# Performance work log

Measured on AMD Instinct MI355X. Metric: run time of the kernel, lower is better.

The kernel has to match this reference:

```python
import jax, jax.numpy as jnp
import numpy as np

B, N, S, D, ITERS = 128, 8192, 4, 32, 3
LN_EPS = 1e-5

def _ln(x, g, b):
    m = jnp.mean(x, axis=-1, keepdims=True)
    v = jnp.mean((x - m) ** 2, axis=-1, keepdims=True)
    return (x - m) * jax.lax.rsqrt(v + LN_EPS) * g + b

def setup_inputs() -> dict:
    key = jax.random.key(0)
    ks = jax.random.split(key, 16)
    s = 1.0 / np.sqrt(D)
    return {
        "x": jax.random.normal(ks[0], (B, N, D), jnp.float32),
        "slot_noise": jax.random.normal(ks[1], (B, S, D), jnp.float32),
        "slots_mu": jax.random.normal(ks[2], (1, 1, D), jnp.float32),
        "slots_logsigma": jnp.zeros((1, 1, D), jnp.float32),
        "Wq": jax.random.uniform(ks[3], (D, D), jnp.float32, -s, s),
        "Wk": jax.random.uniform(ks[4], (D, D), jnp.float32, -s, s),
        "Wv": jax.random.uniform(ks[5], (D, D), jnp.float32, -s, s),
        "gru_Wih": jax.random.uniform(ks[6], (3 * D, D), jnp.float32, -s, s),
        "gru_Whh": jax.random.uniform(ks[7], (3 * D, D), jnp.float32, -s, s),
        "gru_bih": jax.random.uniform(ks[8], (3 * D,), jnp.float32, -s, s),
        "gru_bhh": jax.random.uniform(ks[9], (3 * D,), jnp.float32, -s, s),
        "mlp_W1": jax.random.uniform(ks[10], (D, D), jnp.float32, -s, s),
        "mlp_b1": jax.random.uniform(ks[11], (D,), jnp.float32, -s, s),
        "mlp_W2": jax.random.uniform(ks[12], (D, D), jnp.float32, -s, s),
        "mlp_b2": jax.random.uniform(ks[13], (D,), jnp.float32, -s, s),
        "lnx_g": jnp.ones((D,), jnp.float32), "lnx_b": jnp.zeros((D,), jnp.float32),
        "lns_g": jnp.ones((D,), jnp.float32), "lns_b": jnp.zeros((D,), jnp.float32),
        "lnff_g": jnp.ones((D,), jnp.float32), "lnff_b": jnp.zeros((D,), jnp.float32),
    }

def reference(x, slot_noise, slots_mu, slots_logsigma, Wq, Wk, Wv,
              gru_Wih, gru_Whh, gru_bih, gru_bhh,
              mlp_W1, mlp_b1, mlp_W2, mlp_b2,
              lnx_g, lnx_b, lns_g, lns_b, lnff_g, lnff_b):
    d = x.shape[-1]
    scale = d ** (-0.5)
    xn = _ln(x, lnx_g, lnx_b)                      # [B,N,D]
    k = xn @ Wk.T                                  # [B,N,D] (x fixed -> hoist out of loop)
    v = xn @ Wv.T
    slots = slots_mu + slot_noise * jnp.exp(slots_logsigma)  # [B,S,D]
    for _ in range(ITERS):
        q = _ln(slots, lns_g, lns_b) @ Wq.T        # [B,S,D]
        attn = jnp.einsum('bsd,bnd->bsn', q, k) * scale
        attn = jax.nn.softmax(attn, axis=-1) + 1e-8
        attn = attn / jnp.sum(attn, axis=-1, keepdims=True)
        upd = jnp.einsum('bsn,bnd->bsd', attn, v)  # [B,S,D]
        # GRUCell (PyTorch gate order: r, z, n)
        gi = upd @ gru_Wih.T + gru_bih             # [B,S,3D]
        gh = slots @ gru_Whh.T + gru_bhh
        ir, iz, inn = jnp.split(gi, 3, axis=-1)
        hr, hz, hn = jnp.split(gh, 3, axis=-1)
        r = jax.nn.sigmoid(ir + hr)
        z = jax.nn.sigmoid(iz + hz)
        n = jnp.tanh(inn + r * hn)
        slots = (1.0 - z) * n + z * slots
        h = jax.nn.relu(_ln(slots, lnff_g, lnff_b) @ mlp_W1.T + mlp_b1)
        slots = slots + (h @ mlp_W2.T + mlp_b2)
    return slots.reshape(slots.shape[0], -1)
```

## Files before the change

kernel.cpp:

```cpp
#include <hip/hip_runtime.h>
#include <hip/hip_bf16.h>


#define Bn 128
#define Nn 8192
#define Sn 4
#define Dn 32
#define SCALE 0.17677669529663687f
#define RENORM (1.0f / (1.0f + (float)Nn * 1e-8f))

#define Cn 8
#define RPB (Nn / Cn)
#define PT 256
#define RSTEP 128
#define NSTEP (RPB / RSTEP)

#define WS_REQ ((size_t)(3 * Bn * Sn * Dn + 3 * Bn * Cn * Sn * Dn + 6 * Bn * Cn * Sn) * 4)

__device__ __forceinline__ float sigmoidf_(float v) { return 1.0f / (1.0f + __expf(-v)); }

template<int KIND, int WANT_QT>
__device__ __forceinline__ void chain_fn(
    int b, int tid,
    const float* __restrict__ pa_prev, const float* __restrict__ pb_prev,
    const float* __restrict__ ps_prev,
    const float* __restrict__ slots_prev,
    const float* __restrict__ noise, const float* __restrict__ mu,
    const float* __restrict__ logsig,
    const float* __restrict__ lnx_g, const float* __restrict__ lnx_b,
    const float* __restrict__ Wv,
    const float* __restrict__ Wih, const float* __restrict__ Whh,
    const float* __restrict__ bih, const float* __restrict__ bhh,
    const float* __restrict__ W1, const float* __restrict__ b1v,
    const float* __restrict__ W2, const float* __restrict__ b2v,
    const float* __restrict__ lns_g, const float* __restrict__ lns_b,
    const float* __restrict__ lnff_g, const float* __restrict__ lnff_b,
    const float* __restrict__ Wq, const float* __restrict__ Wk,
    float (*qt_sh)[Dn], float (*ta)[Dn], float (*tb)[Dn],
    float* __restrict__ store)
{
    const int s = (tid >> 5) & 3, d = tid & 31;
    const bool act = tid < 128;
    float sfin = 0.f;

    if constexpr (KIND == 0) {
        if (act)
            sfin = mu[d] + noise[(b * Sn + s) * Dn + d] * __expf(logsig[d]);
    } else {
        float sv_c = 0.f, lnffv = 0.f;
        if (act) {
            float PA = 0.f, PB = 0.f, PS = 0.f;
            #pragma unroll
            for (int c = 0; c < Cn; ++c) {
                PA += pa_prev[(((size_t)b * Cn + c) * Sn + s) * Dn + d];
                PB += pb_prev[((size_t)b * Cn + c) * Sn + s];
                PS += ps_prev[((size_t)b * Cn + c) * Sn + s];
            }
            float u = fmaf(lnx_g[d], PA - PB, PS * lnx_b[d]);
            ta[s][d] = (u / PS) * RENORM;
            tb[s][d] = slots_prev[(b * Sn + s) * Dn + d];
        }
        __syncthreads();
        float updv = 0.f;
        if (act) {
            #pragma unroll 8
            for (int j = 0; j < 32; ++j) updv = fmaf(Wv[d * 32 + j], ta[s][j], updv);
        }
        __syncthreads();
        if (act) ta[s][d] = updv;
        __syncthreads();
        if (act) {
            float gi[3], gh[3];
            #pragma unroll
            for (int g3 = 0; g3 < 3; ++g3) {
                const int row = g3 * 32 + d;
                float a1 = bih[row], a2 = bhh[row];
                #pragma unroll 8
                for (int j = 0; j < 32; ++j) {
                    a1 = fmaf(Wih[row * 32 + j], ta[s][j], a1);
                    a2 = fmaf(Whh[row * 32 + j], tb[s][j], a2);
                }
                gi[g3] = a1; gh[g3] = a2;
            }
            float r  = sigmoidf_(gi[0] + gh[0]);
            float z  = sigmoidf_(gi[1] + gh[1]);
            float nn = tanhf(gi[2] + r * gh[2]);
            sv_c = (1.0f - z) * nn + z * tb[s][d];
            float sx = sv_c, sxx = sv_c * sv_c;
            #pragma unroll
            for (int m = 1; m <= 16; m <<= 1) { sx += __shfl_xor(sx, m); sxx += __shfl_xor(sxx, m); }
            float mean = sx * (1.0f / 32.0f);
            float var  = sxx * (1.0f / 32.0f) - mean * mean;
            lnffv = (sv_c - mean) * rsqrtf(var + 1e-5f) * lnff_g[d] + lnff_b[d];
        }
        __syncthreads();
        if (act) ta[s][d] = lnffv;
        __syncthreads();
        if (act) {
            float h = b1v[d];
            #pragma unroll 8
            for (int j = 0; j < 32; ++j) h = fmaf(W1[d * 32 + j], ta[s][j], h);
            tb[s][d] = fmaxf(h, 0.f);
        }
        __syncthreads();
        if (act) {
            float o = b2v[d];
            #pragma unroll 8
            for (int j = 0; j < 32; ++j) o = fmaf(W2[d * 32 + j], tb[s][j], o);
            sfin = sv_c + o;
        }
    }

    if (act && store) store[(b * Sn + s) * Dn + d] = sfin;

    if constexpr (WANT_QT) {
        float lnsv = 0.f;
        if (act) {
            float sx = sfin, sxx = sfin * sfin;
            #pragma unroll
            for (int m = 1; m <= 16; m <<= 1) { sx += __shfl_xor(sx, m); sxx += __shfl_xor(sxx, m); }
            float mean = sx * (1.0f / 32.0f);
            float var  = sxx * (1.0f / 32.0f) - mean * mean;
            lnsv = (sfin - mean) * rsqrtf(var + 1e-5f) * lns_g[d] + lns_b[d];
        }
        __syncthreads();
        if (act) ta[s][d] = lnsv;
        __syncthreads();
        if (act) {
            float q = 0.f;
            #pragma unroll 8
            for (int j = 0; j < 32; ++j) q = fmaf(Wq[d * 32 + j], ta[s][j], q);
            tb[s][d] = q;
        }
        __syncthreads();
        if (act) {
            float qv = 0.f;
            #pragma unroll 8
            for (int i = 0; i < 32; ++i) qv = fmaf(tb[s][i], Wk[i * 32 + d], qv);
            qt_sh[s][d] = qv * SCALE;
        }
        __syncthreads();
    }
}

template<int IT>
__global__ __launch_bounds__(PT)
void pass_k(const float* __restrict__ x,
            const float* __restrict__ noise, const float* __restrict__ mu,
            const float* __restrict__ logsig,
            const float* __restrict__ Wq, const float* __restrict__ Wk,
            const float* __restrict__ Wv,
            const float* __restrict__ Wih, const float* __restrict__ Whh,
            const float* __restrict__ bih, const float* __restrict__ bhh,
            const float* __restrict__ W1, const float* __restrict__ b1v,
            const float* __restrict__ W2, const float* __restrict__ b2v,
            const float* __restrict__ lnx_g, const float* __restrict__ lnx_b,
            const float* __restrict__ lns_g, const float* __restrict__ lns_b,
            const float* __restrict__ lnff_g, const float* __restrict__ lnff_b,
            const float* __restrict__ slots_prev, float* __restrict__ slots_cur,
            const float* __restrict__ pa_prev, const float* __restrict__ pb_prev,
            const float* __restrict__ ps_prev,
            float* __restrict__ pa_cur, float* __restrict__ pb_cur,
            float* __restrict__ ps_cur)
{
    const int c = blockIdx.x, b = blockIdx.y, tid = threadIdx.x;
    __shared__ float qt_sh[Sn][Dn], ta[Sn][Dn], tb[Sn][Dn];
    __shared__ float ls_pa[4][Sn][Dn];
    __shared__ float ls_pb[4][Sn];
    __shared__ float ls_ps[4][Sn];

    chain_fn<(IT == 0 ? 0 : 1), 1>(b, tid, pa_prev, pb_prev, ps_prev, slots_prev,
        noise, mu, logsig, lnx_g, lnx_b, Wv, Wih, Whh, bih, bhh, W1, b1v, W2, b2v,
        lns_g, lns_b, lnff_g, lnff_b, Wq, Wk,
        qt_sh, ta, tb, (c == 0) ? slots_cur : nullptr);

    const int sub = tid & 3, col0 = sub * 8, rg = tid >> 2;

    float qg[4][8], qgs[4], qe[4];
    {
        float g8[8], e8[8];
        #pragma unroll
        for (int k = 0; k < 8; ++k) { g8[k] = lnx_g[col0 + k]; e8[k] = lnx_b[col0 + k]; }
        #pragma unroll
        for (int s = 0; s < 4; ++s) {
            float sg = 0.f, se = 0.f;
            #pragma unroll
            for (int k = 0; k < 8; ++k) {
                float q = qt_sh[s][col0 + k];
                qg[s][k] = q * g8[k];
                sg += qg[s][k];
                se = fmaf(q, e8[k], se);
            }
            sg += __shfl_xor(sg, 1); sg += __shfl_xor(sg, 2);
            se += __shfl_xor(se, 1); se += __shfl_xor(se, 2);
            qgs[s] = sg; qe[s] = se;
        }
    }

    float pa[4][8], pb[4] = {0.f,0.f,0.f,0.f}, ps[4] = {0.f,0.f,0.f,0.f};
    #pragma unroll
    for (int s = 0; s < 4; ++s)
        #pragma unroll
        for (int k = 0; k < 8; ++k) pa[s][k] = 0.f;

    const float* xb = x + ((size_t)b * Nn + (size_t)c * RPB) * Dn;
    const float* pA0 = xb + (size_t)rg * Dn + col0;
    const float* pB0 = pA0 + 64 * Dn;
    float4 a0 = *(const float4*)(pA0);
    float4 a1 = *(const float4*)(pA0 + 4);
    float4 b0 = *(const float4*)(pB0);
    float4 b1 = *(const float4*)(pB0 + 4);

    for (int t = 0; t < NSTEP; ++t) {
        const int tn = (t + 1 < NSTEP) ? t + 1 : t;
        const float* qA = xb + (size_t)(tn * RSTEP + rg) * Dn + col0;
        const float* qB = qA + 64 * Dn;
        float4 nA0 = *(const float4*)(qA);
        float4 nA1 = *(const float4*)(qA + 4);
        float4 nB0 = *(const float4*)(qB);
        float4 nB1 = *(const float4*)(qB + 4);

        float xA[8] = {a0.x, a0.y, a0.z, a0.w, a1.x, a1.y, a1.z, a1.w};
        float xB[8] = {b0.x, b0.y, b0.z, b0.w, b1.x, b1.y, b1.z, b1.w};

        float sxA = 0.f, sxxA = 0.f, dA[4] = {0.f,0.f,0.f,0.f};
        float sxB = 0.f, sxxB = 0.f, dB[4] = {0.f,0.f,0.f,0.f};
        #pragma unroll
        for (int k = 0; k < 8; ++k) {
            sxA += xA[k];  sxxA = fmaf(xA[k], xA[k], sxxA);
            sxB += xB[k];  sxxB = fmaf(xB[k], xB[k], sxxB);
            #pragma unroll
            for (int s = 0; s < 4; ++s) {
                dA[s] = fmaf(xA[k], qg[s][k], dA[s]);
                dB[s] = fmaf(xB[k], qg[s][k], dB[s]);
            }
        }
        sxA += __shfl_xor(sxA, 1); sxxA += __shfl_xor(sxxA, 1);
        sxB += __shfl_xor(sxB, 1); sxxB += __shfl_xor(sxxB, 1);
        #pragma unroll
        for (int s = 0; s < 4; ++s) { dA[s] += __shfl_xor(dA[s], 1); dB[s] += __shfl_xor(dB[s], 1); }
        sxA += __shfl_xor(sxA, 2); sxxA += __shfl_xor(sxxA, 2);
        sxB += __shfl_xor(sxB, 2); sxxB += __shfl_xor(sxxB, 2);
        #pragma unroll
        for (int s = 0; s < 4; ++s) { dA[s] += __shfl_xor(dA[s], 2); dB[s] += __shfl_xor(dB[s], 2); }

        float meanA = sxA * (1.0f / 32.0f);
        float varA  = sxxA * (1.0f / 32.0f) - meanA * meanA;
        float rsA   = rsqrtf(varA + 1e-5f);
        float meanB = sxB * (1.0f / 32.0f);
        float varB  = sxxB * (1.0f / 32.0f) - meanB * meanB;
        float rsB   = rsqrtf(varB + 1e-5f);

        #pragma unroll
        for (int s = 0; s < 4; ++s) {
            float lgA = fmaf(rsA, fmaf(-meanA, qgs[s], dA[s]), qe[s]);
            float lgB = fmaf(rsB, fmaf(-meanB, qgs[s], dB[s]), qe[s]);
            float wA = __expf(lgA), wB = __expf(lgB);
            float alA = wA * rsA,  alB = wB * rsB;
            ps[s] += wA + wB;
            pb[s] = fmaf(alA, meanA, fmaf(alB, meanB, pb[s]));
            #pragma unroll
            for (int k = 0; k < 8; ++k)
                pa[s][k] = fmaf(alA, xA[k], fmaf(alB, xB[k], pa[s][k]));
        }
        a0 = nA0; a1 = nA1; b0 = nB0; b1 = nB1;
    }

    #pragma unroll
    for (int m = 4; m <= 32; m <<= 1) {
        #pragma unroll
        for (int s = 0; s < 4; ++s) {
            ps[s] += __shfl_xor(ps[s], m);
            pb[s] += __shfl_xor(pb[s], m);
            #pragma unroll
            for (int k = 0; k < 8; ++k) pa[s][k] += __shfl_xor(pa[s][k], m);
        }
    }

    const int wv = tid >> 6, lane = tid & 63;
    if (lane < 4) {
        #pragma unroll
        for (int s = 0; s < 4; ++s)
            #pragma unroll
            for (int k = 0; k < 8; ++k) ls_pa[wv][s][lane * 8 + k] = pa[s][k];
        if (lane == 0) {
            #pragma unroll
            for (int s = 0; s < 4; ++s) { ls_pb[wv][s] = pb[s]; ls_ps[wv][s] = ps[s]; }
        }
    }
    __syncthreads();
    if (tid < 128) {
        const int s = tid >> 5, d = tid & 31;
        float a = ls_pa[0][s][d] + ls_pa[1][s][d] + ls_pa[2][s][d] + ls_pa[3][s][d];
        pa_cur[(((size_t)b * Cn + c) * Sn + s) * Dn + d] = a;
        if (d == 0) {
            pb_cur[((size_t)b * Cn + c) * Sn + s] =
                ls_pb[0][s] + ls_pb[1][s] + ls_pb[2][s] + ls_pb[3][s];
            ps_cur[((size_t)b * Cn + c) * Sn + s] =
                ls_ps[0][s] + ls_ps[1][s] + ls_ps[2][s] + ls_ps[3][s];
        }
    }
}

__global__ __launch_bounds__(128)
void final_k(const float* __restrict__ lnx_g, const float* __restrict__ lnx_b,
             const float* __restrict__ Wv,
             const float* __restrict__ Wih, const float* __restrict__ Whh,
             const float* __restrict__ bih, const float* __restrict__ bhh,
             const float* __restrict__ W1, const float* __restrict__ b1v,
             const float* __restrict__ W2, const float* __restrict__ b2v,
             const float* __restrict__ lns_g, const float* __restrict__ lns_b,
             const float* __restrict__ lnff_g, const float* __restrict__ lnff_b,
             const float* __restrict__ Wq, const float* __restrict__ Wk,
             const float* __restrict__ slots_prev,
             const float* __restrict__ pa_prev, const float* __restrict__ pb_prev,
             const float* __restrict__ ps_prev,
             float* __restrict__ out)
{
    const int b = blockIdx.x, tid = threadIdx.x;
    __shared__ float qt_sh[Sn][Dn], ta[Sn][Dn], tb[Sn][Dn];
    chain_fn<1, 0>(b, tid, pa_prev, pb_prev, ps_prev, slots_prev,
        nullptr, nullptr, nullptr, lnx_g, lnx_b,
        Wv, Wih, Whh, bih, bhh, W1, b1v, W2, b2v,
        lns_g, lns_b, lnff_g, lnff_b, Wq, Wk, qt_sh, ta, tb, out);
}

#define TPB 1024
#define NW (TPB / 64)
#define RPS (TPB / 4)
#define STEPS (Nn / RPS)

__global__ __launch_bounds__(TPB)
void slot_fused(const float* __restrict__ x, const float* __restrict__ noise,
                const float* __restrict__ mu, const float* __restrict__ logsig,
                const float* __restrict__ Wq, const float* __restrict__ Wk,
                const float* __restrict__ Wv,
                const float* __restrict__ Wih, const float* __restrict__ Whh,
                const float* __restrict__ bih, const float* __restrict__ bhh,
                const float* __restrict__ W1, const float* __restrict__ b1v,
                const float* __restrict__ W2, const float* __restrict__ b2v,
                const float* __restrict__ lnx_g, const float* __restrict__ lnx_b,
                const float* __restrict__ lns_g, const float* __restrict__ lns_b,
                const float* __restrict__ lnff_g, const float* __restrict__ lnff_b,
                float* __restrict__ out)
{
    const int b   = blockIdx.x;
    const int tid = threadIdx.x;
    __shared__ float slots_sh[Sn][Dn];
    __shared__ float qt_sh[Sn][Dn];
    __shared__ float a_sh[Sn][Dn];
    __shared__ float b_sh[Sn][Dn];
    __shared__ float h_sh[Sn][Dn];
    __shared__ float ls_u[NW][Sn][Dn];
    __shared__ float ls_s[NW][Sn];
    const int s128 = tid >> 5, d128 = tid & 31;

    if (tid < 128) {
        float sv = mu[d128] + noise[(b * Sn + s128) * Dn + d128] * __expf(logsig[d128]);
        slots_sh[s128][d128] = sv;
        float sx = sv, sxx = sv * sv;
        #pragma unroll
        for (int m = 1; m <= 16; m <<= 1) { sx += __shfl_xor(sx, m); sxx += __shfl_xor(sxx, m); }
        float mean = sx * (1.0f / 32.0f);
        float var  = sxx * (1.0f / 32.0f) - mean * mean;
        a_sh[s128][d128] = (sv - mean) * rsqrtf(var + 1e-5f) * lns_g[d128] + lns_b[d128];
    }
    __syncthreads();
    if (tid < 128) {
        float q = 0.f;
        #pragma unroll 8
        for (int j = 0; j < 32; ++j) q = fmaf(Wq[d128 * 32 + j], a_sh[s128][j], q);
        b_sh[s128][d128] = q;
    }
    __syncthreads();
    if (tid < 128) {
        float qv = 0.f;
        #pragma unroll 8
        for (int i = 0; i < 32; ++i) qv = fmaf(b_sh[s128][i], Wk[i * 32 + d128], qv);
        qt_sh[s128][d128] = qv * SCALE;
    }
    __syncthreads();

    const int sub = tid & 3, col0 = sub * 8;
    const int rg  = tid >> 2;
    float g_r[8], e_r[8];
    #pragma unroll
    for (int k = 0; k < 8; ++k) { g_r[k] = lnx_g[col0 + k]; e_r[k] = lnx_b[col0 + k]; }
    const float* xb = x + (size_t)b * Nn * Dn;
    float sv_reg = 0.f;

    for (int it = 0; it < 3; ++it) {
        float qt_r[4][8];
        #pragma unroll
        for (int s = 0; s < 4; ++s)
            #pragma unroll
            for (int k = 0; k < 8; ++k) qt_r[s][k] = qt_sh[s][col0 + k];
        float pu[4][8];
        float ps[4] = {0.f, 0.f, 0.f, 0.f};
        #pragma unroll
        for (int s = 0; s < 4; ++s)
            #pragma unroll
            for (int k = 0; k < 8; ++k) pu[s][k] = 0.f;

        const float* xr0 = xb + (size_t)rg * Dn + col0;
        float4 v0 = *(const float4*)(xr0);
        float4 v1 = *(const float4*)(xr0 + 4);
        #pragma unroll 2
        for (int t = 0; t < STEPS; ++t) {
            const float* xrn = xb + (size_t)((((t + 1) & (STEPS - 1)) * RPS) + rg) * Dn + col0;
            float4 n0 = *(const float4*)(xrn);
            float4 n1 = *(const float4*)(xrn + 4);
            float xv[8] = {v0.x, v0.y, v0.z, v0.w, v1.x, v1.y, v1.z, v1.w};
            float sx = 0.f, sxx = 0.f;
            #pragma unroll
            for (int k = 0; k < 8; ++k) { sx += xv[k]; sxx = fmaf(xv[k], xv[k], sxx); }
            sx += __shfl_xor(sx, 1); sxx += __shfl_xor(sxx, 1);
            sx += __shfl_xor(sx, 2); sxx += __shfl_xor(sxx, 2);
            float mean = sx * (1.0f / 32.0f);
            float var  = sxx * (1.0f / 32.0f) - mean * mean;
            float rs   = rsqrtf(var + 1e-5f);
            float xn[8];
            #pragma unroll
            for (int k = 0; k < 8; ++k) xn[k] = fmaf((xv[k] - mean) * rs, g_r[k], e_r[k]);
            #pragma unroll
            for (int s = 0; s < 4; ++s) {
                float a = 0.f;
                #pragma unroll
                for (int k = 0; k < 8; ++k) a = fmaf(xn[k], qt_r[s][k], a);
                a += __shfl_xor(a, 1);
                a += __shfl_xor(a, 2);
                float w = __expf(a);
                ps[s] += w;
                #pragma unroll
                for (int k = 0; k < 8; ++k) pu[s][k] = fmaf(w, xn[k], pu[s][k]);
            }
            v0 = n0; v1 = n1;
        }
        #pragma unroll
        for (int m = 4; m <= 32; m <<= 1) {
            #pragma unroll
            for (int s = 0; s < 4; ++s) {
                ps[s] += __shfl_xor(ps[s], m);
                #pragma unroll
                for (int k = 0; k < 8; ++k) pu[s][k] += __shfl_xor(pu[s][k], m);
            }
        }
        {
            const int wv = tid >> 6, lane = tid & 63;
            if (lane < 4) {
                #pragma unroll
                for (int s = 0; s < 4; ++s)
                    #pragma unroll
                    for (int k = 0; k < 8; ++k) ls_u[wv][s][lane * 8 + k] = pu[s][k];
                if (lane == 0) {
                    #pragma unroll
                    for (int s = 0; s < 4; ++s) ls_s[wv][s] = ps[s];
                }
            }
        }
        __syncthreads();
        if (tid < 128) {
            float u = 0.f, ss = 0.f;
            #pragma unroll
            for (int w = 0; w < NW; ++w) { u += ls_u[w][s128][d128]; ss += ls_s[w][s128]; }
            a_sh[s128][d128] = (u / ss) * RENORM;
        }
        __syncthreads();
        if (tid < 128) {
            float upd = 0.f;
            #pragma unroll 8
            for (int j = 0; j < 32; ++j) upd = fmaf(Wv[d128 * 32 + j], a_sh[s128][j], upd);
            b_sh[s128][d128] = upd;
        }
        __syncthreads();
        if (tid < 128) {
            float gi[3], gh[3];
            #pragma unroll
            for (int g3 = 0; g3 < 3; ++g3) {
                const int row = g3 * 32 + d128;
                float a1 = bih[row], a2 = bhh[row];
                #pragma unroll 8
                for (int j = 0; j < 32; ++j) {
                    a1 = fmaf(Wih[row * 32 + j], b_sh[s128][j], a1);
                    a2 = fmaf(Whh[row * 32 + j], slots_sh[s128][j], a2);
                }
                gi[g3] = a1; gh[g3] = a2;
            }
            float r  = sigmoidf_(gi[0] + gh[0]);
            float z  = sigmoidf_(gi[1] + gh[1]);
            float nn = tanhf(gi[2] + r * gh[2]);
            sv_reg = (1.0f - z) * nn + z * slots_sh[s128][d128];
            float sx = sv_reg, sxx = sv_reg * sv_reg;
            #pragma unroll
            for (int m = 1; m <= 16; m <<= 1) { sx += __shfl_xor(sx, m); sxx += __shfl_xor(sxx, m); }
            float mean = sx * (1.0f / 32.0f);
            float var  = sxx * (1.0f / 32.0f) - mean * mean;
            a_sh[s128][d128] = (sv_reg - mean) * rsqrtf(var + 1e-5f) * lnff_g[d128] + lnff_b[d128];
        }
        __syncthreads();
        if (tid < 128) {
            float h = b1v[d128];
            #pragma unroll 8
            for (int j = 0; j < 32; ++j) h = fmaf(W1[d128 * 32 + j], a_sh[s128][j], h);
            h_sh[s128][d128] = fmaxf(h, 0.f);
        }
        __syncthreads();
        if (tid < 128) {
            float o = b2v[d128];
            #pragma unroll 8
            for (int j = 0; j < 32; ++j) o = fmaf(W2[d128 * 32 + j], h_sh[s128][j], o);
            float sfin = sv_reg + o;
            slots_sh[s128][d128] = sfin;
            if (it < 2) {
                float sx = sfin, sxx = sfin * sfin;
                #pragma unroll
                for (int m = 1; m <= 16; m <<= 1) { sx += __shfl_xor(sx, m); sxx += __shfl_xor(sxx, m); }
                float mean = sx * (1.0f / 32.0f);
                float var  = sxx * (1.0f / 32.0f) - mean * mean;
                a_sh[s128][d128] = (sfin - mean) * rsqrtf(var + 1e-5f) * lns_g[d128] + lns_b[d128];
            }
        }
        __syncthreads();
        if (it < 2) {
            if (tid < 128) {
                float q = 0.f;
                #pragma unroll 8
                for (int j = 0; j < 32; ++j) q = fmaf(Wq[d128 * 32 + j], a_sh[s128][j], q);
                b_sh[s128][d128] = q;
            }
            __syncthreads();
            if (tid < 128) {
                float qv = 0.f;
                #pragma unroll 8
                for (int i = 0; i < 32; ++i) qv = fmaf(b_sh[s128][i], Wk[i * 32 + d128], qv);
                qt_sh[s128][d128] = qv * SCALE;
            }
            __syncthreads();
        }
    }
    if (tid < 128)
        out[(size_t)b * 128 + tid] = slots_sh[s128][d128];
}

extern "C" void kernel_launch(void* const* d_in, const int* in_sizes, int n_in,
                              void* d_out, int out_size, void* d_ws, size_t ws_size,
                              hipStream_t stream)
{
    const float* x      = (const float*)d_in[0];
    const float* noise  = (const float*)d_in[1];
    const float* mu     = (const float*)d_in[2];
    const float* logsig = (const float*)d_in[3];
    const float* Wq     = (const float*)d_in[4];
    const float* Wk     = (const float*)d_in[5];
    const float* Wv     = (const float*)d_in[6];
    const float* Wih    = (const float*)d_in[7];
    const float* Whh    = (const float*)d_in[8];
    const float* bih    = (const float*)d_in[9];
    const float* bhh    = (const float*)d_in[10];
    const float* W1     = (const float*)d_in[11];
    const float* b1v    = (const float*)d_in[12];
    const float* W2     = (const float*)d_in[13];
    const float* b2v    = (const float*)d_in[14];
    const float* lnx_g  = (const float*)d_in[15];
    const float* lnx_b  = (const float*)d_in[16];
    const float* lns_g  = (const float*)d_in[17];
    const float* lns_b  = (const float*)d_in[18];
    const float* lnff_g = (const float*)d_in[19];
    const float* lnff_b = (const float*)d_in[20];
    float* out = (float*)d_out;

    if (ws_size >= WS_REQ) {
        float* wsf    = (float*)d_ws;
        float* slots0 = wsf;
        float* slots1 = slots0 + Bn * Sn * Dn;
        float* slots2 = slots1 + Bn * Sn * Dn;
        float* pa0    = slots2 + Bn * Sn * Dn;
        float* pa1    = pa0 + Bn * Cn * Sn * Dn;
        float* pa2    = pa1 + Bn * Cn * Sn * Dn;
        float* pb0    = pa2 + Bn * Cn * Sn * Dn;
        float* pb1    = pb0 + Bn * Cn * Sn;
        float* pb2    = pb1 + Bn * Cn * Sn;
        float* ps0    = pb2 + Bn * Cn * Sn;
        float* ps1    = ps0 + Bn * Cn * Sn;
        float* ps2    = ps1 + Bn * Cn * Sn;

        pass_k<0><<<dim3(Cn, Bn), PT, 0, stream>>>(x, noise, mu, logsig,
            Wq, Wk, Wv, Wih, Whh, bih, bhh, W1, b1v, W2, b2v,
            lnx_g, lnx_b, lns_g, lns_b, lnff_g, lnff_b,
            nullptr, slots0, nullptr, nullptr, nullptr, pa0, pb0, ps0);
        pass_k<1><<<dim3(Cn, Bn), PT, 0, stream>>>(x, noise, mu, logsig,
            Wq, Wk, Wv, Wih, Whh, bih, bhh, W1, b1v, W2, b2v,
            lnx_g, lnx_b, lns_g, lns_b, lnff_g, lnff_b,
            slots0, slots1, pa0, pb0, ps0, pa1, pb1, ps1);
        pass_k<2><<<dim3(Cn, Bn), PT, 0, stream>>>(x, noise, mu, logsig,
            Wq, Wk, Wv, Wih, Whh, bih, bhh, W1, b1v, W2, b2v,
            lnx_g, lnx_b, lns_g, lns_b, lnff_g, lnff_b,
            slots1, slots2, pa1, pb1, ps1, pa2, pb2, ps2);
        final_k<<<Bn, 128, 0, stream>>>(lnx_g, lnx_b, Wv, Wih, Whh, bih, bhh,
            W1, b1v, W2, b2v, lns_g, lns_b, lnff_g, lnff_b, Wq, Wk,
            slots2, pa2, pb2, ps2, out);
    } else {
        slot_fused<<<Bn, TPB, 0, stream>>>(x, noise, mu, logsig, Wq, Wk, Wv,
                                           Wih, Whh, bih, bhh, W1, b1v, W2, b2v,
                                           lnx_g, lnx_b, lns_g, lns_b, lnff_g, lnff_b,
                                           out);
    }
}
```

Measured before the change: 135.5 us.

## Stage x chunk in padded LDS and split rows across more blocks

The row dimension is split across 32 blocks per batch instead of 8, and each block first loads its 256-row chunk of x into padded shared memory with coalesced float4 loads. It then runs the fully unrolled LayerNorm/softmax accumulation loop from LDS, replacing the register double-buffered global loads. This is meant to raise parallelism and hide global latency through a bulk prefetch. In exchange it uses about 37KB of LDS per block, which may limit occupancy, and produces four times as many partial sums to reduce.

```diff
diff --git a/kernel.cpp b/kernel.cpp
--- a/kernel.cpp
+++ b/kernel.cpp
@@ -9,11 +9,10 @@
 #define SCALE 0.17677669529663687f
 #define RENORM (1.0f / (1.0f + (float)Nn * 1e-8f))
 
-#define Cn 8
+#define Cn 32
 #define RPB (Nn / Cn)
 #define PT 256
-#define RSTEP 128
-#define NSTEP (RPB / RSTEP)
+#define LSTR 9
 
 #define WS_REQ ((size_t)(3 * Bn * Sn * Dn + 3 * Bn * Cn * Sn * Dn + 6 * Bn * Cn * Sn) * 4)
 
@@ -164,6 +163,7 @@
             float* __restrict__ ps_cur)
 {
     const int c = blockIdx.x, b = blockIdx.y, tid = threadIdx.x;
+    __shared__ float4 xls[RPB * LSTR];
     __shared__ float qt_sh[Sn][Dn], ta[Sn][Dn], tb[Sn][Dn];
     __shared__ float ls_pa[4][Sn][Dn];
     __shared__ float ls_pb[4][Sn];
@@ -173,6 +173,19 @@
         noise, mu, logsig, lnx_g, lnx_b, Wv, Wih, Whh, bih, bhh, W1, b1v, W2, b2v,
         lns_g, lns_b, lnff_g, lnff_b, Wq, Wk,
         qt_sh, ta, tb, (c == 0) ? slots_cur : nullptr);
+
+    {
+        const float4* src = (const float4*)(x + ((size_t)b * Nn + (size_t)c * RPB) * Dn);
+        float4 st[8];
+        #pragma unroll
+        for (int i = 0; i < 8; ++i) st[i] = src[tid + (i << 8)];
+        #pragma unroll
+        for (int i = 0; i < 8; ++i) {
+            const int f = tid + (i << 8);
+            xls[(f >> 3) * LSTR + (f & 7)] = st[i];
+        }
+    }
+    __syncthreads();
 
     const int sub = tid & 3, col0 = sub * 8, rg = tid >> 2;
 
@@ -203,67 +216,42 @@
         #pragma unroll
         for (int k = 0; k < 8; ++k) pa[s][k] = 0.f;
 
-    const float* xb = x + ((size_t)b * Nn + (size_t)c * RPB) * Dn;
-    const float* pA0 = xb + (size_t)rg * Dn + col0;
-    const float* pB0 = pA0 + 64 * Dn;
-    float4 a0 = *(const float4*)(pA0);
-    float4 a1 = *(const float4*)(pA0 + 4);
-    float4 b0 = *(const float4*)(pB0);
-    float4 b1 = *(const float4*)(pB0 + 4);
-
-    for (int t = 0; t < NSTEP; ++t) {
-        const int tn = (t + 1 < NSTEP) ? t + 1 : t;
-        const float* qA = xb + (size_t)(tn * RSTEP + rg) * Dn + col0;
-        const float* qB = qA + 64 * Dn;
-        float4 nA0 = *(const float4*)(qA);
-        float4 nA1 = *(const float4*)(qA + 4);
-        float4 nB0 = *(const float4*)(qB);
-        float4 nB1 = *(const float4*)(qB + 4);
-
-        float xA[8] = {a0.x, a0.y, a0.z, a0.w, a1.x, a1.y, a1.z, a1.w};
-        float xB[8] = {b0.x, b0.y, b0.z, b0.w, b1.x, b1.y, b1.z, b1.w};
-
-        float sxA = 0.f, sxxA = 0.f, dA[4] = {0.f,0.f,0.f,0.f};
-        float sxB = 0.f, sxxB = 0.f, dB[4] = {0.f,0.f,0.f,0.f};
+    #pragma unroll
+    for (int t = 0; t < RPB / 64; ++t) {
+        const int row = t * 64 + rg;
+        const float4 v0 = xls[row * LSTR + sub * 2];
+        const float4 v1 = xls[row * LSTR + sub * 2 + 1];
+        float xv[8] = {v0.x, v0.y, v0.z, v0.w, v1.x, v1.y, v1.z, v1.w};
+
+        float sx = 0.f, sxx = 0.f, ds[4] = {0.f,0.f,0.f,0.f};
         #pragma unroll
         for (int k = 0; k < 8; ++k) {
-            sxA += xA[k];  sxxA = fmaf(xA[k], xA[k], sxxA);
-            sxB += xB[k];  sxxB = fmaf(xB[k], xB[k], sxxB);
-            #pragma unroll
-            for (int s = 0; s < 4; ++s) {
-                dA[s] = fmaf(xA[k], qg[s][k], dA[s]);
-                dB[s] = fmaf(xB[k], qg[s][k], dB[s]);
-            }
-        }
-        sxA += __shfl_xor(sxA, 1); sxxA += __shfl_xor(sxxA, 1);
-        sxB += __shfl_xor(sxB, 1); sxxB += __shfl_xor(sxxB, 1);
-        #pragma unroll
-        for (int s = 0; s < 4; ++s) { dA[s] += __shfl_xor(dA[s], 1); dB[s] += __shfl_xor(dB[s], 1); }
-        sxA += __shfl_xor(sxA, 2); sxxA += __shfl_xor(sxxA, 2);
-        sxB += __shfl_xor(sxB, 2); sxxB += __shfl_xor(sxxB, 2);
-        #pragma unroll
-        for (int s = 0; s < 4; ++s) { dA[s] += __shfl_xor(dA[s], 2); dB[s] += __shfl_xor(dB[s], 2); }
-
-        float meanA = sxA * (1.0f / 32.0f);
-        float varA  = sxxA * (1.0f / 32.0f) - meanA * meanA;
-        float rsA   = rsqrtf(varA + 1e-5f);
-        float meanB = sxB * (1.0f / 32.0f);
-        float varB  = sxxB * (1.0f / 32.0f) - meanB * meanB;
-        float rsB   = rsqrtf(varB + 1e-5f);
+            sx += xv[k];
+            sxx = fmaf(xv[k], xv[k], sxx);
+            #pragma unroll
+            for (int s = 0; s < 4; ++s) ds[s] = fmaf(xv[k], qg[s][k], ds[s]);
+        }
+        sx += __shfl_xor(sx, 1); sxx += __shfl_xor(sxx, 1);
+        #pragma unroll
+        for (int s = 0; s < 4; ++s) ds[s] += __shfl_xor(ds[s], 1);
+        sx += __shfl_xor(sx, 2); sxx += __shfl_xor(sxx, 2);
+        #pragma unroll
+        for (int s = 0; s < 4; ++s) ds[s] += __shfl_xor(ds[s], 2);
+
+        float mean = sx * (1.0f / 32.0f);
+        float var  = sxx * (1.0f / 32.0f) - mean * mean;
+        float rs   = rsqrtf(var + 1e-5f);
 
         #pragma unroll
         for (int s = 0; s < 4; ++s) {
-            float lgA = fmaf(rsA, fmaf(-meanA, qgs[s], dA[s]), qe[s]);
-            float lgB = fmaf(rsB, fmaf(-meanB, qgs[s], dB[s]), qe[s]);
-            float wA = __expf(lgA), wB = __expf(lgB);
-            float alA = wA * rsA,  alB = wB * rsB;
-            ps[s] += wA + wB;
-            pb[s] = fmaf(alA, meanA, fmaf(alB, meanB, pb[s]));
-            #pragma unroll
-            for (int k = 0; k < 8; ++k)
-                pa[s][k] = fmaf(alA, xA[k], fmaf(alB, xB[k], pa[s][k]));
-        }
-        a0 = nA0; a1 = nA1; b0 = nB0; b1 = nB1;
+            float lg = fmaf(rs, fmaf(-mean, qgs[s], ds[s]), qe[s]);
+            float w  = __expf(lg);
+            float al = w * rs;
+            ps[s] += w;
+            pb[s] = fmaf(al, mean, pb[s]);
+            #pragma unroll
+            for (int k = 0; k < 8; ++k) pa[s][k] = fmaf(al, xv[k], pa[s][k]);
+        }
     }
 
     #pragma unroll
```

Result: slower. 292.0 us (+115.5%).
